# Optimization experiments

Hardware: AMD Instinct MI355X
Metric: run time of the kernel (lower is better)

Reference implementation:

```python
import jax, jax.numpy as jnp
import numpy as np
import math

FS = 44100.0
HOP = 256
N_BANDS = 24
KS_BUF = 768  # > max delay 44100/60 = 735 samples


def _lpc1(x, a):
    # order-1 all-pole (sample_wise_lpc with order 1, per-batch constant coeff):
    # y[n] = x[n] - a*y[n-1];  x: [B,N], a: [B]
    def step(yp, xt):
        y = xt - a * yp
        return y, y
    _, ys = jax.lax.scan(step, jnp.zeros_like(a), x.T)
    return ys.T


def _diff_ks(f0_frames, exc, l_b):
    # differentiable Karplus-Strong: fractional-delay loop + 2-tap damping filter.
    # f0_frames: [B,F] Hz, exc: [B,N], l_b: [B,F,2] (loop_coeff, loop_mix logits)
    B, N = exc.shape
    g = 0.999 * jax.nn.sigmoid(l_b[..., 0])   # loop gain in (0, 0.999)
    s = jax.nn.sigmoid(l_b[..., 1])           # loop-filter mix
    up = lambda p: jnp.repeat(p, HOP, axis=1)[:, :N]
    g_s, s_s = up(g), up(s)
    f0_s = up(jnp.clip(f0_frames, 60.0, None))
    D = jnp.clip(FS / f0_s, 2.0, 735.0)        # delay in samples
    Di = jnp.floor(D).astype(jnp.int32)
    fr = (D - Di).astype(exc.dtype)
    L = KS_BUF

    def step(carry, xs):
        buf, n = carry                         # buf: [B,L] circular delay line
        x_t, Di_t, fr_t, g_t, s_t = xs         # each [B]
        i1 = jnp.mod(n - Di_t, L)
        i2 = jnp.mod(n - Di_t - 1, L)
        i3 = jnp.mod(n - Di_t - 2, L)
        take = lambda i: jnp.take_along_axis(buf, i[:, None], axis=1)[:, 0]
        b1, b2, b3 = take(i1), take(i2), take(i3)
        z = (1.0 - fr_t) * b1 + fr_t * b2      # fractional-delay read y[n-D]
        z1 = (1.0 - fr_t) * b2 + fr_t * b3     # y[n-D-1]
        y = x_t + g_t * ((1.0 - s_t) * z + s_t * z1)
        buf = buf.at[:, jnp.mod(n, L)].set(y)
        return (buf, n + 1), y

    xs = (exc.T, Di.T, fr.T, g_s.T, s_s.T)
    init = (jnp.zeros((B, L), exc.dtype), jnp.int32(0))
    _, ys = jax.lax.scan(step, init, xs)
    return ys.T


def _body(x, body_gains):
    # bank of 24 two-pole resonators, log-spaced 80..8000 Hz, Q=10
    fc = jnp.geomspace(80.0, 8000.0, N_BANDS).astype(x.dtype)
    w = 2.0 * jnp.pi * fc / FS
    r = jnp.exp(-jnp.pi * fc / (10.0 * FS))
    a1 = -2.0 * r * jnp.cos(w)
    a2 = r * r
    b0 = 1.0 - r
    B = x.shape[0]

    def step(carry, xt):
        y1, y2 = carry                          # [B,24] each
        y = b0 * xt[:, None] - a1 * y1 - a2 * y2
        return (y, y1), jnp.sum(y * body_gains, axis=-1)

    init = (jnp.zeros((B, N_BANDS), x.dtype), jnp.zeros((B, N_BANDS), x.dtype))
    _, out = jax.lax.scan(step, init, x.T)
    return out.T


def _forward(excitation, pitch, w1, b1, w2, b2, excitation_gain, body_gains):
    B, _, N = excitation.shape
    h = jax.nn.relu(pitch @ w1.T + b1)
    mlp_out = h @ w2.T + b2                     # [B,3]
    loop_coeff = jnp.clip(mlp_out[:, 0], -2.0, 2.5)
    loop_mix = jnp.clip(mlp_out[:, 1], -2.5, 0.0)
    frames = N // HOP
    l_b = jnp.broadcast_to(jnp.stack([loop_coeff, loop_mix], -1)[:, None, :], (B, frames, 2))
    f0_frames = jnp.broadcast_to(pitch, (B, frames))
    exc_sq = (excitation * excitation_gain)[:, 0, :]
    f0_hz = jnp.clip(pitch[:, 0], 60.0, None)
    mult = jnp.clip(2.0 + 6.0 * (f0_hz - 60.0) / 600.0, 2.0, 8.0)
    cutoff = jnp.minimum(2.0 * jnp.pi * f0_hz * mult / FS, jnp.pi * 0.9)
    alpha = 1.0 - jnp.exp(-cutoff)
    exc_f = _lpc1(exc_sq * alpha[:, None], alpha - 1.0)   # pre-KS one-pole LP
    string = _diff_ks(f0_frames, exc_f, l_b)
    loop_post = jnp.clip(mlp_out[:, 2], -4.0, 4.0)
    cutoff_post = jnp.minimum(jnp.pi * jax.nn.sigmoid(loop_post), jnp.pi * 0.99)
    alpha_p = 1.0 - jnp.exp(-cutoff_post)
    string = _lpc1(string * alpha_p[:, None], alpha_p - 1.0)  # post one-pole LP
    out = _body(string, body_gains)
    return out[:, None, :], loop_coeff.mean(), loop_mix.mean(), loop_post.mean()


def setup_inputs():
    key = jax.random.key(0)
    k = jax.random.split(key, 6)
    B, N = 8, 32768
    excitation = jax.random.normal(k[0], (B, 1, N), dtype=jnp.float32)
    pitch = 60.0 + 600.0 * jax.random.uniform(k[1], (B, 1), dtype=jnp.float32)
    bnd1 = 0.1 * math.sqrt(6.0 / (1 + 16))   # xavier_uniform, gain 0.1
    bnd2 = 0.1 * math.sqrt(6.0 / (16 + 3))
    w1 = jax.random.uniform(k[2], (16, 1), jnp.float32, -bnd1, bnd1)
    b1 = jnp.zeros((16,), jnp.float32)
    w2 = jax.random.uniform(k[3], (3, 16), jnp.float32, -bnd2, bnd2)
    b2 = jnp.array([0.9, 0.0, 0.0], jnp.float32)
    excitation_gain = jnp.array(0.25, jnp.float32)
    body_gains = 0.006 * jnp.ones((1, N_BANDS), jnp.float32)
    return {"excitation": excitation, "pitch": pitch, "w1": w1, "b1": b1,
            "w2": w2, "b2": b2, "excitation_gain": excitation_gain,
            "body_gains": body_gains}


def reference(excitation, pitch, w1, b1, w2, b2, excitation_gain, body_gains):
    return _forward(excitation, pitch, w1, b1, w2, b2, excitation_gain, body_gains)
```

## Files before the change

### kernel.cpp

```cpp
#include <hip/hip_runtime.h>
#include <math.h>

#define NSAMP 32768
#define FS_F 44100.0f
#define PI_F 3.14159265358979323846f
#define T1 1024
#define FLAG_MAGIC 0x5A5A5A5A

struct BParams {
  float alpha, alpha_p;
  float fr, g, s;
  int Di;
  float lc, lm, lp;
};

__device__ inline float sigmoidf_(float x) { return 1.0f / (1.0f + expf(-x)); }

__device__ inline BParams compute_params(int b, const float* __restrict__ pitch,
                                         const float* __restrict__ w1,
                                         const float* __restrict__ b1,
                                         const float* __restrict__ w2,
                                         const float* __restrict__ b2) {
  BParams P;
  float p = pitch[b];
  float h[16];
#pragma unroll
  for (int i = 0; i < 16; ++i) {
    float v = fmaf(p, w1[i], b1[i]);
    h[i] = v > 0.0f ? v : 0.0f;
  }
  float m[3];
#pragma unroll
  for (int j = 0; j < 3; ++j) {
    float acc = b2[j];
#pragma unroll
    for (int i = 0; i < 16; ++i) acc = fmaf(h[i], w2[j * 16 + i], acc);
    m[j] = acc;
  }
  P.lc = fminf(fmaxf(m[0], -2.0f), 2.5f);
  P.lm = fminf(fmaxf(m[1], -2.5f), 0.0f);
  P.lp = fminf(fmaxf(m[2], -4.0f), 4.0f);
  P.g = 0.999f * sigmoidf_(P.lc);
  P.s = sigmoidf_(P.lm);
  float f0 = fmaxf(p, 60.0f);
  float D = fminf(fmaxf(FS_F / f0, 2.0f), 735.0f);
  int Di = (int)floorf(D);
  P.fr = D - (float)Di;
  P.Di = Di;
  float mult = fminf(fmaxf(2.0f + 6.0f * (f0 - 60.0f) / 600.0f, 2.0f), 8.0f);
  float cutoff = fminf(2.0f * PI_F * f0 * mult / FS_F, PI_F * 0.9f);
  P.alpha = 1.0f - expf(-cutoff);
  float cpost = fminf(PI_F * sigmoidf_(P.lp), PI_F * 0.99f);
  P.alpha_p = 1.0f - expf(-cpost);
  return P;
}

__device__ inline float rl63(float v) {
  return __int_as_float(__builtin_amdgcn_readlane(__float_as_int(v), 63));
}
__device__ inline float rlv(float v, int l) {
  return __int_as_float(__builtin_amdgcn_readlane(__float_as_int(v), l));
}
__device__ inline float shr1(float v, float bnd) {
  return __int_as_float(__builtin_amdgcn_update_dpp(
      __float_as_int(bnd), __float_as_int(v), 0x138 , 0xf, 0xf,
      false));
}

__device__ inline void barrier_lgkm() {
  asm volatile("s_waitcnt lgkmcnt(0)\n\ts_barrier" ::: "memory");
}

__device__ inline void band_coef(int k, float& a1, float& a2, float& b0) {
  float fc = 80.0f * exp2f((float)k * (6.64385618977472436f / 23.0f));
  float w = 2.0f * PI_F * fc / FS_F;
  float r = expf(-PI_F * fc / (10.0f * FS_F));
  a1 = -2.0f * r * cosf(w);
  a2 = r * r;
  b0 = 1.0f - r;
}

struct SCtx {
  const float* exc_b;
  float scale, c;
  float m1, m2, m4, m8, m16, m32, c512, c2048, c8lane, cgk;
  float vrun;
  int s1;
  float* lws;
};

__device__ inline void scan_seg(SCtx& SC, float* xbuf, int seg, bool write,
                                int t) {
  const int lane = t & 63, wid = t >> 6;
  const int rel0 = seg << 11;
  const int A = SC.s1 + rel0;
  __syncthreads();
  const int g0 = A + 8 * t;
  float4 xa = make_float4(0.f, 0.f, 0.f, 0.f);
  float4 xb = make_float4(0.f, 0.f, 0.f, 0.f);
  if (g0 >= 0 && g0 + 3 < NSAMP) xa = *(const float4*)&SC.exc_b[g0];
  if (g0 + 4 >= 0 && g0 + 7 < NSAMP) xb = *(const float4*)&SC.exc_b[g0 + 4];
  const float c = SC.c, scale = SC.scale;
  float S = 0.0f;
  S = fmaf(c, S, scale * xa.x); S = fmaf(c, S, scale * xa.y);
  S = fmaf(c, S, scale * xa.z); S = fmaf(c, S, scale * xa.w);
  S = fmaf(c, S, scale * xb.x); S = fmaf(c, S, scale * xb.y);
  S = fmaf(c, S, scale * xb.z); S = fmaf(c, S, scale * xb.w);
  float Sw = S, u;
  u = __shfl_up(Sw, 1);  if (lane >= 1)  Sw = fmaf(SC.m1, u, Sw);
  u = __shfl_up(Sw, 2);  if (lane >= 2)  Sw = fmaf(SC.m2, u, Sw);
  u = __shfl_up(Sw, 4);  if (lane >= 4)  Sw = fmaf(SC.m4, u, Sw);
  u = __shfl_up(Sw, 8);  if (lane >= 8)  Sw = fmaf(SC.m8, u, Sw);
  u = __shfl_up(Sw, 16); if (lane >= 16) Sw = fmaf(SC.m16, u, Sw);
  u = __shfl_up(Sw, 32); if (lane >= 32) Sw = fmaf(SC.m32, u, Sw);
  if (lane == 63) SC.lws[wid] = Sw;
  __syncthreads();
  float a0 = SC.lws[0], a1w = SC.lws[1], a2w = SC.lws[2], a3w = SC.lws[3];
  float carry = (wid == 1)   ? a0
                : (wid == 2) ? fmaf(SC.c512, a0, a1w)
                : (wid == 3) ? fmaf(SC.c512, fmaf(SC.c512, a0, a1w), a2w)
                             : 0.0f;
  float Sprev = __shfl_up(Sw, 1);
  float Sex = (lane == 0) ? 0.0f : Sprev;
  Sex = fmaf(SC.c8lane, carry, Sex);
  float v = fmaf(SC.cgk, SC.vrun, Sex);
  float4 ya, yb;
  v = fmaf(c, v, scale * xa.x); ya.x = v;
  v = fmaf(c, v, scale * xa.y); ya.y = v;
  v = fmaf(c, v, scale * xa.z); ya.z = v;
  v = fmaf(c, v, scale * xa.w); ya.w = v;
  v = fmaf(c, v, scale * xb.x); yb.x = v;
  v = fmaf(c, v, scale * xb.y); yb.y = v;
  v = fmaf(c, v, scale * xb.z); yb.z = v;
  v = fmaf(c, v, scale * xb.w); yb.w = v;
  if (write) {
    int o = (rel0 + 8 * t) & 8191;
    *(float4*)&xbuf[o] = ya;
    *(float4*)&xbuf[o + 4] = yb;
  }
  float tS = fmaf(SC.c512, fmaf(SC.c512, fmaf(SC.c512, a0, a1w), a2w), a3w);
  SC.vrun = fmaf(SC.c2048, SC.vrun, tS);
}

template <int KNUM>
__device__ void ks_slice2(SCtx& SC, float* __restrict__ yg, float* xbuf,
                          float* bnd, int t, int C, float c0w, float c1w,
                          float c2w, int s1, int n0, int end, int span,
                          int nseg) {
  const int lane = t & 63;
  const int wid = t >> 6;
  const int lq1 = (C - 1) - (KNUM - 1) * 64;
  const int W = n0 - s1;

  if (KNUM <= 3) {
    float yp[KNUM], xC[KNUM], xN[KNUM], xN2[KNUM];
    float p1 = 0.f, p2 = 0.f;
    int rel = 0;
#pragma unroll
    for (int k = 0; k < KNUM; ++k) {
      yp[k] = 0.f; xC[k] = 0.f; xN[k] = 0.f; xN2[k] = 0.f;
    }
    for (int s = 0; s < nseg; ++s) {
      barrier_lgkm();
      if (wid == 0) {
        if (s == 0) {
#pragma unroll
          for (int k = 0; k < KNUM; ++k) {
            int i = lane + (k << 6);
            xC[k] = xbuf[i];
            xN[k] = xbuf[C + i];
            xN2[k] = xbuf[2 * C + i];
          }
        }
        int fence = (s + 1) << 11;
        if (fence > span) fence = span;
        while (rel + C <= W && rel < fence) {
          float b2v[KNUM], b3v[KNUM];
#pragma unroll
          for (int k = 0; k < KNUM; ++k)
            b2v[k] = shr1(yp[k], (k == 0) ? p1 : rl63(yp[k - 1]));
#pragma unroll
          for (int k = 0; k < KNUM; ++k)
            b3v[k] = shr1(b2v[k], (k == 0) ? p2 : rlv(yp[k - 1], 62));
          float p1n = rlv(yp[KNUM - 1], lq1);
          float p2n = rlv(b2v[KNUM - 1], lq1);
#pragma unroll
          for (int k = 0; k < KNUM; ++k)
            yp[k] = fmaf(c0w, yp[k],
                         fmaf(c2w, b3v[k], fmaf(c1w, b2v[k], xC[k])));
          p1 = p1n;
          p2 = p2n;
#pragma unroll
          for (int k = 0; k < KNUM; ++k) {
            xC[k] = xN[k];
            xN[k] = xN2[k];
            xN2[k] = xbuf[(rel + 3 * C + lane + (k << 6)) & 8191];
          }
          rel += C;
        }
        while (rel < fence) {
          float b2v[KNUM], b3v[KNUM];
#pragma unroll
          for (int k = 0; k < KNUM; ++k)
            b2v[k] = shr1(yp[k], (k == 0) ? p1 : rl63(yp[k - 1]));
#pragma unroll
          for (int k = 0; k < KNUM; ++k)
            b3v[k] = shr1(b2v[k], (k == 0) ? p2 : rlv(yp[k - 1], 62));
          float p1n = rlv(yp[KNUM - 1], lq1);
          float p2n = rlv(b2v[KNUM - 1], lq1);
#pragma unroll
          for (int k = 0; k < KNUM; ++k)
            yp[k] = fmaf(c0w, yp[k],
                         fmaf(c2w, b3v[k], fmaf(c1w, b2v[k], xC[k])));
          p1 = p1n;
          p2 = p2n;
#pragma unroll
          for (int k = 0; k < KNUM; ++k) {
            int i = lane + (k << 6);
            int n = s1 + rel + i;
            bool okl = (k < KNUM - 1) || (lane <= lq1);
            if (okl && n >= n0 && n < end) yg[n] = yp[k];
          }
#pragma unroll
          for (int k = 0; k < KNUM; ++k) {
            xC[k] = xN[k];
            xN[k] = xN2[k];
            xN2[k] = xbuf[(rel + 3 * C + lane + (k << 6)) & 8191];
          }
          rel += C;
        }
      }
      barrier_lgkm();
      int ls = s + 3;
      if (ls < nseg) scan_seg(SC, xbuf, ls, true, t);
    }
  } else {
    constexpr int SPW = (KNUM + 3) / 4;
    const int kbase = wid * SPW;
    float yp[SPW], xC[SPW], xN[SPW], xN2[SPW];
    int rel = 0, par = 0;
#pragma unroll
    for (int kk = 0; kk < SPW; ++kk) {
      yp[kk] = 0.f; xC[kk] = 0.f; xN[kk] = 0.f; xN2[kk] = 0.f;
    }
    for (int s = 0; s < nseg; ++s) {
      barrier_lgkm();
      if (s == 0) {
#pragma unroll
        for (int kk = 0; kk < SPW; ++kk) {
          int k = kbase + kk;
          if (k < KNUM) {
            int i = lane + (k << 6);
            xC[kk] = xbuf[i];
            xN[kk] = xbuf[C + i];
            xN2[kk] = xbuf[2 * C + i];
          }
        }
      }
      int fence = (s + 1) << 11;
      if (fence > span) fence = span;
      while (rel < fence) {
        const bool lean = (rel + C <= W);
        barrier_lgkm();
        const int rb = par << 5, wb = rb ^ 32;
        float pbA = 0.f, pbB = 0.f;
        if (kbase == 0) {
          pbA = bnd[rb + 24];
          pbB = bnd[rb + 25];
        } else if (kbase < KNUM) {
          pbA = bnd[rb + (kbase - 1) * 2];
          pbB = bnd[rb + (kbase - 1) * 2 + 1];
        }
        float b2v[SPW], b3v[SPW];
#pragma unroll
        for (int kk = 0; kk < SPW; ++kk) {
          int k = kbase + kk;
          if (k < KNUM)
            b2v[kk] = shr1(yp[kk], (kk == 0) ? pbA : rl63(yp[kk - 1]));
        }
#pragma unroll
        for (int kk = 0; kk < SPW; ++kk) {
          int k = kbase + kk;
          if (k < KNUM)
            b3v[kk] = shr1(b2v[kk], (kk == 0) ? pbB : rlv(yp[kk - 1], 62));
        }
        float p1n = 0.f, p2n = 0.f;
        const bool ownLast = (KNUM - 1 >= kbase) && (KNUM - 1 < kbase + SPW);
        if (ownLast) {
          p1n = rlv(yp[KNUM - 1 - kbase], lq1);
          p2n = rlv(b2v[KNUM - 1 - kbase], lq1);
        }
#pragma unroll
        for (int kk = 0; kk < SPW; ++kk) {
          int k = kbase + kk;
          if (k < KNUM)
            yp[kk] = fmaf(c0w, yp[kk],
                          fmaf(c2w, b3v[kk], fmaf(c1w, b2v[kk], xC[kk])));
        }
        if (!lean) {
#pragma unroll
          for (int kk = 0; kk < SPW; ++kk) {
            int k = kbase + kk;
            if (k < KNUM) {
              int i = lane + (k << 6);
              int n = s1 + rel + i;
              bool okl = (k < KNUM - 1) || (lane <= lq1);
              if (okl && n >= n0 && n < end) yg[n] = yp[kk];
            }
          }
        }
#pragma unroll
        for (int kk = 0; kk < SPW; ++kk) {
          int k = kbase + kk;
          if (k < KNUM) {
            float h63 = rlv(yp[kk], 63);
            float h62 = rlv(yp[kk], 62);
            if (lane == 0) {
              bnd[wb + k * 2] = h63;
              bnd[wb + k * 2 + 1] = h62;
            }
          }
        }
        if (ownLast && lane == 0) {
          bnd[wb + 24] = p1n;
          bnd[wb + 25] = p2n;
        }
#pragma unroll
        for (int kk = 0; kk < SPW; ++kk) {
          int k = kbase + kk;
          if (k < KNUM) {
            xC[kk] = xN[kk];
            xN[kk] = xN2[kk];
            xN2[kk] = xbuf[(rel + 3 * C + lane + (k << 6)) & 8191];
          }
        }
        rel += C;
        par ^= 1;
      }
      barrier_lgkm();
      int ls = s + 3;
      if (ls < nseg) scan_seg(SC, xbuf, ls, true, t);
    }
  }
}

__device__ inline void lpc_lds(const float* __restrict__ xg,
                               float* __restrict__ sl, int s2, int nt, int lim,
                               float scale, float c, int t, float* lws) {
  const int lane = t & 63, wid = t >> 6;
  float c2v = c * c, c4 = c2v * c2v, c8 = c4 * c4;
  float m1 = c8, m2 = m1 * m1, m4 = m2 * m2, m8 = m4 * m4, m16 = m8 * m8,
        m32 = m16 * m16;
  float c512 = m32 * m32;
  float c2048 = c512 * c512;
  c2048 *= c2048;
  float l2c = log2f(c);
  float c8lane = exp2f((float)(8 * lane) * l2c);
  float cgk = exp2f((float)(8 * t) * l2c);
  float vrun = 0.0f;
  for (int tile = 0; tile < nt; ++tile) {
    __syncthreads();
    int g0 = s2 + (tile << 11) + 8 * t;
    float4 xa = make_float4(0.f, 0.f, 0.f, 0.f);
    float4 xb = make_float4(0.f, 0.f, 0.f, 0.f);
    if (g0 + 3 < lim) xa = *(const float4*)&xg[g0];
    if (g0 + 7 < lim) xb = *(const float4*)&xg[g0 + 4];
    float S = 0.0f;
    S = fmaf(c, S, scale * xa.x); S = fmaf(c, S, scale * xa.y);
    S = fmaf(c, S, scale * xa.z); S = fmaf(c, S, scale * xa.w);
    S = fmaf(c, S, scale * xb.x); S = fmaf(c, S, scale * xb.y);
    S = fmaf(c, S, scale * xb.z); S = fmaf(c, S, scale * xb.w);
    float Sw = S, u;
    u = __shfl_up(Sw, 1);  if (lane >= 1)  Sw = fmaf(m1, u, Sw);
    u = __shfl_up(Sw, 2);  if (lane >= 2)  Sw = fmaf(m2, u, Sw);
    u = __shfl_up(Sw, 4);  if (lane >= 4)  Sw = fmaf(m4, u, Sw);
    u = __shfl_up(Sw, 8);  if (lane >= 8)  Sw = fmaf(m8, u, Sw);
    u = __shfl_up(Sw, 16); if (lane >= 16) Sw = fmaf(m16, u, Sw);
    u = __shfl_up(Sw, 32); if (lane >= 32) Sw = fmaf(m32, u, Sw);
    if (lane == 63) lws[wid] = Sw;
    __syncthreads();
    float a0 = lws[0], a1w = lws[1], a2w = lws[2], a3w = lws[3];
    float carry = (wid == 1)   ? a0
                  : (wid == 2) ? fmaf(c512, a0, a1w)
                  : (wid == 3) ? fmaf(c512, fmaf(c512, a0, a1w), a2w)
                               : 0.0f;
    float Sprev = __shfl_up(Sw, 1);
    float Sex = (lane == 0) ? 0.0f : Sprev;
    Sex = fmaf(c8lane, carry, Sex);
    float v = fmaf(cgk, vrun, Sex);
    int o = g0 - s2;
    float4 ya, yb;
    v = fmaf(c, v, scale * xa.x); ya.x = v;
    v = fmaf(c, v, scale * xa.y); ya.y = v;
    v = fmaf(c, v, scale * xa.z); ya.z = v;
    v = fmaf(c, v, scale * xa.w); ya.w = v;
    v = fmaf(c, v, scale * xb.x); yb.x = v;
    v = fmaf(c, v, scale * xb.y); yb.y = v;
    v = fmaf(c, v, scale * xb.z); yb.z = v;
    v = fmaf(c, v, scale * xb.w); yb.w = v;
    *(float4*)&sl[o] = ya;
    *(float4*)&sl[o + 4] = yb;
    float tS = fmaf(c512, fmaf(c512, fmaf(c512, a0, a1w), a2w), a3w);
    vrun = fmaf(c2048, vrun, tS);
  }
}

__device__ inline void ks_phase(int b, int q, const BParams& P,
                                const float* __restrict__ exc, float scale0,
                                float* __restrict__ buf1, float* xbuf,
                                float* bnd, float* lws, int t) {
  const int C = P.Di;
  const int n0 = q << 10;
  float lg = -logf(P.g);
  int Wp = (int)ceilf(10.5f / fmaxf(lg, 1e-6f));
  if (Wp > 64) Wp = 64;
  if (Wp < 4) Wp = 4;
  int W = Wp * C;
  if (W > n0) W = n0;
  W = (W + 3) & ~3;
  const int s1 = n0 - W;
  const int span = W + T1;
  const int end = n0 + T1;
  const int nseg = (span + 2047) >> 11;
  float* yg = buf1 + (size_t)b * NSAMP;

  SCtx SC;
  SC.exc_b = exc + (size_t)b * NSAMP;
  SC.c = 1.0f - P.alpha;
  SC.scale = scale0 * P.alpha;
  {
    float c = SC.c;
    float c2v = c * c, c4 = c2v * c2v, c8 = c4 * c4;
    SC.m1 = c8;
    SC.m2 = SC.m1 * SC.m1;
    SC.m4 = SC.m2 * SC.m2;
    SC.m8 = SC.m4 * SC.m4;
    SC.m16 = SC.m8 * SC.m8;
    SC.m32 = SC.m16 * SC.m16;
    SC.c512 = SC.m32 * SC.m32;
    float c1024 = SC.c512 * SC.c512;
    SC.c2048 = c1024 * c1024;
    float l2c = log2f(c);
    SC.c8lane = exp2f((float)(8 * (t & 63)) * l2c);
    SC.cgk = exp2f((float)(8 * t) * l2c);
  }
  SC.vrun = 0.0f;
  SC.s1 = s1;
  SC.lws = lws;

  if (s1 > 0) scan_seg(SC, xbuf, -1, false, t);
  scan_seg(SC, xbuf, 0, true, t);
  scan_seg(SC, xbuf, 1, true, t);
  scan_seg(SC, xbuf, 2, true, t);
  if (t < 64) bnd[t] = 0.0f;

  const float c0w = P.g * (1.0f - P.s) * (1.0f - P.fr);
  const float c1w = P.g * ((1.0f - P.s) * P.fr + P.s * (1.0f - P.fr));
  const float c2w = P.g * P.s * P.fr;
  switch ((C + 63) >> 6) {
    case 2:  ks_slice2<2>(SC, yg, xbuf, bnd, t, C, c0w, c1w, c2w, s1, n0, end, span, nseg); break;
    case 3:  ks_slice2<3>(SC, yg, xbuf, bnd, t, C, c0w, c1w, c2w, s1, n0, end, span, nseg); break;
    case 4:  ks_slice2<4>(SC, yg, xbuf, bnd, t, C, c0w, c1w, c2w, s1, n0, end, span, nseg); break;
    case 5:  ks_slice2<5>(SC, yg, xbuf, bnd, t, C, c0w, c1w, c2w, s1, n0, end, span, nseg); break;
    case 6:  ks_slice2<6>(SC, yg, xbuf, bnd, t, C, c0w, c1w, c2w, s1, n0, end, span, nseg); break;
    case 7:  ks_slice2<7>(SC, yg, xbuf, bnd, t, C, c0w, c1w, c2w, s1, n0, end, span, nseg); break;
    case 8:  ks_slice2<8>(SC, yg, xbuf, bnd, t, C, c0w, c1w, c2w, s1, n0, end, span, nseg); break;
    case 9:  ks_slice2<9>(SC, yg, xbuf, bnd, t, C, c0w, c1w, c2w, s1, n0, end, span, nseg); break;
    case 10: ks_slice2<10>(SC, yg, xbuf, bnd, t, C, c0w, c1w, c2w, s1, n0, end, span, nseg); break;
    case 11: ks_slice2<11>(SC, yg, xbuf, bnd, t, C, c0w, c1w, c2w, s1, n0, end, span, nseg); break;
    default: ks_slice2<12>(SC, yg, xbuf, bnd, t, C, c0w, c1w, c2w, s1, n0, end, span, nseg); break;
  }
}

__device__ inline void body_phase(int b, int q, const BParams& P,
                                  const float* __restrict__ gains,
                                  const float* __restrict__ buf1,
                                  float* __restrict__ out, float* sl,
                                  float* lws, float (*lc0)[8],
                                  float (*lc1)[8], int t) {
  const int lane = t & 63, wid = t >> 6;
  const int n0 = q << 10;
  const int base = n0 - 4096;
  int s2 = base - 256;
  if (s2 < 0) s2 = 0;
  const int end = n0 + 1024;
  const int nt = (end - s2 + 2047) >> 11;

  lpc_lds(buf1 + (size_t)b * NSAMP, sl, s2, nt, end, P.alpha_p,
          1.0f - P.alpha_p, t, lws);
  __syncthreads();

  const int tb = base + 20 * t;
  float4 acc[5];
#pragma unroll
  for (int i = 0; i < 5; ++i) acc[i] = make_float4(0.f, 0.f, 0.f, 0.f);

  for (int g = 0; g < 3; ++g) {
    float A1[8], A2[8], B0[8], GN[8];
#pragma unroll
    for (int j = 0; j < 8; ++j) {
      int k = g * 8 + j;
      band_coef(k, A1[j], A2[j], B0[j]);
      GN[j] = gains[k];
    }
    float cv0[8], cv1[8];
#pragma unroll
    for (int j = 0; j < 8; ++j) cv0[j] = cv1[j] = 0.f;
    for (int i = 0; i < 5; ++i) {
      int n = tb + 4 * i;
      float4 xv = make_float4(0.f, 0.f, 0.f, 0.f);
      if (n >= 0) xv = *(const float4*)&sl[n - s2];
#pragma unroll
      for (int e = 0; e < 4; ++e) {
        float xi = e == 0 ? xv.x : e == 1 ? xv.y : e == 2 ? xv.z : xv.w;
#pragma unroll
        for (int j = 0; j < 8; ++j) {
          float nc = fmaf(B0[j], xi, -fmaf(A1[j], cv0[j], A2[j] * cv1[j]));
          cv1[j] = cv0[j];
          cv0[j] = nc;
        }
      }
    }
    float Q00[8], Q01[8], Q10[8], Q11[8];
    float K00[8], K01[8], K10[8], K11[8];
#pragma unroll
    for (int j = 0; j < 8; ++j) {
      Q00[j] = -A1[j]; Q01[j] = -A2[j]; Q10[j] = 1.f; Q11[j] = 0.f;
    }
    for (int sq = 0; sq < 2; ++sq) {
#pragma unroll
      for (int j = 0; j < 8; ++j) {
        float n00 = fmaf(Q00[j], Q00[j], Q01[j] * Q10[j]);
        float n01 = fmaf(Q00[j], Q01[j], Q01[j] * Q11[j]);
        float n10 = fmaf(Q10[j], Q00[j], Q11[j] * Q10[j]);
        float n11 = fmaf(Q10[j], Q01[j], Q11[j] * Q11[j]);
        Q00[j] = n00; Q01[j] = n01; Q10[j] = n10; Q11[j] = n11;
      }
    }
#pragma unroll
    for (int j = 0; j < 8; ++j) {
      K00[j] = Q00[j]; K01[j] = Q01[j]; K10[j] = Q10[j]; K11[j] = Q11[j];
    }
    for (int sq = 0; sq < 2; ++sq) {
#pragma unroll
      for (int j = 0; j < 8; ++j) {
        float n00 = fmaf(Q00[j], Q00[j], Q01[j] * Q10[j]);
        float n01 = fmaf(Q00[j], Q01[j], Q01[j] * Q11[j]);
        float n10 = fmaf(Q10[j], Q00[j], Q11[j] * Q10[j]);
        float n11 = fmaf(Q10[j], Q01[j], Q11[j] * Q11[j]);
        Q00[j] = n00; Q01[j] = n01; Q10[j] = n10; Q11[j] = n11;
      }
    }
    float T00[8], T01[8], T10[8], T11[8];
#pragma unroll
    for (int j = 0; j < 8; ++j) {
      float n00 = fmaf(Q00[j], K00[j], Q01[j] * K10[j]);
      float n01 = fmaf(Q00[j], K01[j], Q01[j] * K11[j]);
      float n10 = fmaf(Q10[j], K00[j], Q11[j] * K10[j]);
      float n11 = fmaf(Q10[j], K01[j], Q11[j] * K11[j]);
      Q00[j] = n00; Q01[j] = n01; Q10[j] = n10; Q11[j] = n11;
      T00[j] = n00; T01[j] = n01; T10[j] = n10; T11[j] = n11;
    }
    for (int off = 1; off <= 32; off <<= 1) {
#pragma unroll
      for (int j = 0; j < 8; ++j) {
        float u0 = __shfl_up(cv0[j], off);
        float u1 = __shfl_up(cv1[j], off);
        if (lane >= off) {
          float nc0 = fmaf(Q00[j], u0, fmaf(Q01[j], u1, cv0[j]));
          float nc1 = fmaf(Q10[j], u0, fmaf(Q11[j], u1, cv1[j]));
          cv0[j] = nc0;
          cv1[j] = nc1;
        }
        float n00 = fmaf(Q00[j], Q00[j], Q01[j] * Q10[j]);
        float n01 = fmaf(Q00[j], Q01[j], Q01[j] * Q11[j]);
        float n10 = fmaf(Q10[j], Q00[j], Q11[j] * Q10[j]);
        float n11 = fmaf(Q10[j], Q01[j], Q11[j] * Q11[j]);
        Q00[j] = n00; Q01[j] = n01; Q10[j] = n10; Q11[j] = n11;
      }
    }
    __syncthreads();
    if (lane == 63) {
#pragma unroll
      for (int j = 0; j < 8; ++j) {
        lc0[wid][j] = cv0[j];
        lc1[wid][j] = cv1[j];
      }
    }
    __syncthreads();
    float car0[8], car1[8];
#pragma unroll
    for (int j = 0; j < 8; ++j) car0[j] = car1[j] = 0.f;
    for (int v = 0; v < wid; ++v) {
#pragma unroll
      for (int j = 0; j < 8; ++j) {
        float n0c = fmaf(Q00[j], car0[j], fmaf(Q01[j], car1[j], lc0[v][j]));
        float n1c = fmaf(Q10[j], car0[j], fmaf(Q11[j], car1[j], lc1[v][j]));
        car0[j] = n0c;
        car1[j] = n1c;
      }
    }
    float R00[8], R01[8], R10[8], R11[8];
#pragma unroll
    for (int j = 0; j < 8; ++j) {
      R00[j] = 1.f; R01[j] = 0.f; R10[j] = 0.f; R11[j] = 1.f;
    }
    for (int bit = 0; bit < 6; ++bit) {
      bool on = (lane >> bit) & 1;
#pragma unroll
      for (int j = 0; j < 8; ++j) {
        if (on) {
          float n00 = fmaf(T00[j], R00[j], T01[j] * R10[j]);
          float n01 = fmaf(T00[j], R01[j], T01[j] * R11[j]);
          float n10 = fmaf(T10[j], R00[j], T11[j] * R10[j]);
          float n11 = fmaf(T10[j], R01[j], T11[j] * R11[j]);
          R00[j] = n00; R01[j] = n01; R10[j] = n10; R11[j] = n11;
        }
        float s00 = fmaf(T00[j], T00[j], T01[j] * T10[j]);
        float s01 = fmaf(T00[j], T01[j], T01[j] * T11[j]);
        float s10 = fmaf(T10[j], T00[j], T11[j] * T10[j]);
        float s11 = fmaf(T10[j], T01[j], T11[j] * T11[j]);
        T00[j] = s00; T01[j] = s01; T10[j] = s10; T11[j] = s11;
      }
    }
    float y1[8], y2[8];
#pragma unroll
    for (int j = 0; j < 8; ++j) {
      float e0 = __shfl_up(cv0[j], 1);
      float e1 = __shfl_up(cv1[j], 1);
      if (lane == 0) { e0 = 0.f; e1 = 0.f; }
      y1[j] = fmaf(R00[j], car0[j], fmaf(R01[j], car1[j], e0));
      y2[j] = fmaf(R10[j], car0[j], fmaf(R11[j], car1[j], e1));
    }
    if (tb + 20 > n0) {
      for (int i = 0; i < 5; ++i) {
        float4 xv = *(const float4*)&sl[tb - s2 + 4 * i];
        float4 ov = acc[i];
#pragma unroll
        for (int e = 0; e < 4; ++e) {
          float xi = e == 0 ? xv.x : e == 1 ? xv.y : e == 2 ? xv.z : xv.w;
          float a = 0.f;
#pragma unroll
          for (int j = 0; j < 8; ++j) {
            float yv = fmaf(B0[j], xi, -fmaf(A1[j], y1[j], A2[j] * y2[j]));
            y2[j] = y1[j];
            y1[j] = yv;
            a = fmaf(GN[j], yv, a);
          }
          if (e == 0) ov.x += a;
          else if (e == 1) ov.y += a;
          else if (e == 2) ov.z += a;
          else ov.w += a;
        }
        acc[i] = ov;
      }
    }
  }
  if (tb + 20 > n0) {
    float* outb = out + (size_t)b * NSAMP;
#pragma unroll
    for (int i = 0; i < 5; ++i) {
      int n = tb + 4 * i;
      if (n >= n0) *(float4*)&outb[n] = acc[i];
    }
  }
}

__global__ void __launch_bounds__(256, 1) synth_all(
    const float* __restrict__ exc, const float* __restrict__ pitch,
    const float* __restrict__ w1, const float* __restrict__ b1,
    const float* __restrict__ w2, const float* __restrict__ b2,
    const float* __restrict__ eg, const float* __restrict__ gains,
    float* __restrict__ buf1, int* __restrict__ flags,
    float* __restrict__ out) {
  const int blk = blockIdx.x;
  const int b = blk >> 5, q = blk & 31;
  const int t = threadIdx.x;
  __shared__ __align__(16) float smem[8264];

  BParams P = compute_params(b, pitch, w1, b1, w2, b2);
  if (blk == 0 && t < 64) {
    int bb = (t < 8) ? t : 0;
    BParams Q = compute_params(bb, pitch, w1, b1, w2, b2);
    float slc = 0.f, slm = 0.f, slp = 0.f;
    for (int i = 0; i < 8; ++i) {
      slc += rlv(Q.lc, i);
      slm += rlv(Q.lm, i);
      slp += rlv(Q.lp, i);
    }
    if (t == 0) {
      out[8 * NSAMP + 0] = slc / 8.0f;
      out[8 * NSAMP + 1] = slm / 8.0f;
      out[8 * NSAMP + 2] = slp / 8.0f;
    }
  }

  ks_phase(b, q, P, exc, eg[0], buf1, smem, smem + 8192, smem + 8256, t);
  __syncthreads();

  const int n0 = q << 10;
  int s2 = n0 - 4096 - 256;
  if (s2 < 0) s2 = 0;
  const int qlo = s2 >> 10;
  if (t == 0) {
    __hip_atomic_store(&flags[blk], FLAG_MAGIC, __ATOMIC_RELEASE,
                       __HIP_MEMORY_SCOPE_AGENT);
    for (int f = qlo; f < q; ++f) {
      while (__hip_atomic_load(&flags[b * 32 + f], __ATOMIC_ACQUIRE,
                               __HIP_MEMORY_SCOPE_AGENT) != FLAG_MAGIC) {
        __builtin_amdgcn_s_sleep(8);
      }
    }
  }
  __syncthreads();

  body_phase(b, q, P, gains, buf1, out, smem, smem + 6144,
             (float(*)[8])(smem + 6152), (float(*)[8])(smem + 6184), t);
}

extern "C" void kernel_launch(void* const* d_in, const int* in_sizes, int n_in,
                              void* d_out, int out_size, void* d_ws, size_t ws_size,
                              hipStream_t stream) {
  const float* exc = (const float*)d_in[0];
  const float* pitch = (const float*)d_in[1];
  const float* w1 = (const float*)d_in[2];
  const float* b1 = (const float*)d_in[3];
  const float* w2 = (const float*)d_in[4];
  const float* b2 = (const float*)d_in[5];
  const float* eg = (const float*)d_in[6];
  const float* bg = (const float*)d_in[7];
  float* out = (float*)d_out;
  float* buf1 = (float*)d_ws;
  int* flags = (int*)(buf1 + 8 * NSAMP);

  hipLaunchKernelGGL(synth_all, dim3(256), dim3(256), 0, stream, exc, pitch,
                     w1, b1, w2, b2, eg, bg, buf1, flags, out);
}
```

Baseline: 133.5 us.

## Run Karplus-Strong loop on one wave and overlap LPC scan on another

The Karplus-Strong recurrence now always runs inside wave 0, which holds all delay-line slices in registers. This replaces the multi-wave path for long delays, which traded boundary values through LDS with a block barrier every step. Wave 1 computes the order-1 LPC prescan of upcoming segments with a per-wave shuffle scan and prefetched global loads, so it overlaps with the recurrence instead of interleaving block-wide scans. The first four segment loads are issued up front, and the boundary LDS scratch is removed. The cost is that long-delay batches do serial per-lane work on one wave, and waves 2 and 3 sit idle during this phase.

```diff
diff --git a/kernel.cpp b/kernel.cpp
--- a/kernel.cpp
+++ b/kernel.cpp
@@ -89,17 +89,19 @@
   float* lws;
 };
 
-__device__ inline void scan_seg(SCtx& SC, float* xbuf, int seg, bool write,
-                                int t) {
+__device__ inline void ld2(const float* __restrict__ p, int g0, float4& a,
+                           float4& b) {
+  a = make_float4(0.f, 0.f, 0.f, 0.f);
+  b = make_float4(0.f, 0.f, 0.f, 0.f);
+  if (g0 >= 0 && g0 + 3 < NSAMP) a = *(const float4*)&p[g0];
+  if (g0 + 4 >= 0 && g0 + 7 < NSAMP) b = *(const float4*)&p[g0 + 4];
+}
+
+__device__ inline void scan_seg_pre(SCtx& SC, float* xbuf, int seg, bool write,
+                                    int t, float4 xa, float4 xb) {
   const int lane = t & 63, wid = t >> 6;
   const int rel0 = seg << 11;
-  const int A = SC.s1 + rel0;
-  __syncthreads();
-  const int g0 = A + 8 * t;
-  float4 xa = make_float4(0.f, 0.f, 0.f, 0.f);
-  float4 xb = make_float4(0.f, 0.f, 0.f, 0.f);
-  if (g0 >= 0 && g0 + 3 < NSAMP) xa = *(const float4*)&SC.exc_b[g0];
-  if (g0 + 4 >= 0 && g0 + 7 < NSAMP) xb = *(const float4*)&SC.exc_b[g0 + 4];
+  barrier_lgkm();
   const float c = SC.c, scale = SC.scale;
   float S = 0.0f;
   S = fmaf(c, S, scale * xa.x); S = fmaf(c, S, scale * xa.y);
@@ -114,7 +116,7 @@
   u = __shfl_up(Sw, 16); if (lane >= 16) Sw = fmaf(SC.m16, u, Sw);
   u = __shfl_up(Sw, 32); if (lane >= 32) Sw = fmaf(SC.m32, u, Sw);
   if (lane == 63) SC.lws[wid] = Sw;
-  __syncthreads();
+  barrier_lgkm();
   float a0 = SC.lws[0], a1w = SC.lws[1], a2w = SC.lws[2], a3w = SC.lws[3];
   float carry = (wid == 1)   ? a0
                 : (wid == 2) ? fmaf(SC.c512, a0, a1w)
@@ -142,205 +144,221 @@
   SC.vrun = fmaf(SC.c2048, SC.vrun, tS);
 }
 
+__device__ inline void w1_load(const float* __restrict__ xg, int s1, int seg,
+                               int lane, float4* pf) {
+  const int base = s1 + (seg << 11) + (lane << 5);
+#pragma unroll
+  for (int i = 0; i < 8; ++i) {
+    const int g = base + 4 * i;
+    float4 v = make_float4(0.f, 0.f, 0.f, 0.f);
+    if (g >= 0 && g + 3 < NSAMP) v = *(const float4*)&xg[g];
+    pf[i] = v;
+  }
+}
+
 template <int KNUM>
-__device__ void ks_slice2(SCtx& SC, float* __restrict__ yg, float* xbuf,
-                          float* bnd, int t, int C, float c0w, float c1w,
-                          float c2w, int s1, int n0, int end, int span,
-                          int nseg) {
-  const int lane = t & 63;
-  const int wid = t >> 6;
+__device__ void ks_wave0(float* __restrict__ yg, const float* xbuf, int lane,
+                         int C, float c0w, float c1w, float c2w, int s1,
+                         int n0, int end, int span, int nseg) {
   const int lq1 = (C - 1) - (KNUM - 1) * 64;
   const int W = n0 - s1;
-
-  if (KNUM <= 3) {
-    float yp[KNUM], xC[KNUM], xN[KNUM], xN2[KNUM];
-    float p1 = 0.f, p2 = 0.f;
-    int rel = 0;
-#pragma unroll
-    for (int k = 0; k < KNUM; ++k) {
-      yp[k] = 0.f; xC[k] = 0.f; xN[k] = 0.f; xN2[k] = 0.f;
-    }
+  float yp[KNUM], xC[KNUM], xN[KNUM], xN2[KNUM];
+  float p1 = 0.f, p2 = 0.f;
+  int rel = 0;
+#pragma unroll
+  for (int k = 0; k < KNUM; ++k) {
+    yp[k] = 0.f; xC[k] = 0.f; xN[k] = 0.f; xN2[k] = 0.f;
+  }
+  for (int s = 0; s < nseg; ++s) {
+    barrier_lgkm();
+    if (s == 0) {
+#pragma unroll
+      for (int k = 0; k < KNUM; ++k) {
+        int i = lane + (k << 6);
+        xC[k] = xbuf[i];
+        xN[k] = xbuf[C + i];
+        xN2[k] = xbuf[2 * C + i];
+      }
+    }
+    int fence = (s + 1) << 11;
+    if (fence > span) fence = span;
+    while (rel + C <= W && rel < fence) {
+      float b2v[KNUM], b3v[KNUM];
+#pragma unroll
+      for (int k = 0; k < KNUM; ++k)
+        b2v[k] = shr1(yp[k], (k == 0) ? p1 : rl63(yp[k - 1]));
+#pragma unroll
+      for (int k = 0; k < KNUM; ++k)
+        b3v[k] = shr1(b2v[k], (k == 0) ? p2 : rlv(yp[k - 1], 62));
+      float p1n = rlv(yp[KNUM - 1], lq1);
+      float p2n = rlv(b2v[KNUM - 1], lq1);
+#pragma unroll
+      for (int k = 0; k < KNUM; ++k)
+        yp[k] = fmaf(c0w, yp[k], fmaf(c2w, b3v[k], fmaf(c1w, b2v[k], xC[k])));
+      p1 = p1n;
+      p2 = p2n;
+#pragma unroll
+      for (int k = 0; k < KNUM; ++k) {
+        xC[k] = xN[k];
+        xN[k] = xN2[k];
+        xN2[k] = xbuf[(rel + 3 * C + lane + (k << 6)) & 8191];
+      }
+      rel += C;
+    }
+    while (rel < fence) {
+      float b2v[KNUM], b3v[KNUM];
+#pragma unroll
+      for (int k = 0; k < KNUM; ++k)
+        b2v[k] = shr1(yp[k], (k == 0) ? p1 : rl63(yp[k - 1]));
+#pragma unroll
+      for (int k = 0; k < KNUM; ++k)
+        b3v[k] = shr1(b2v[k], (k == 0) ? p2 : rlv(yp[k - 1], 62));
+      float p1n = rlv(yp[KNUM - 1], lq1);
+      float p2n = rlv(b2v[KNUM - 1], lq1);
+#pragma unroll
+      for (int k = 0; k < KNUM; ++k)
+        yp[k] = fmaf(c0w, yp[k], fmaf(c2w, b3v[k], fmaf(c1w, b2v[k], xC[k])));
+      p1 = p1n;
+      p2 = p2n;
+#pragma unroll
+      for (int k = 0; k < KNUM; ++k) {
+        int i = lane + (k << 6);
+        int n = s1 + rel + i;
+        bool okl = (k < KNUM - 1) || (lane <= lq1);
+        if (okl && n >= n0 && n < end) yg[n] = yp[k];
+      }
+#pragma unroll
+      for (int k = 0; k < KNUM; ++k) {
+        xC[k] = xN[k];
+        xN[k] = xN2[k];
+        xN2[k] = xbuf[(rel + 3 * C + lane + (k << 6)) & 8191];
+      }
+      rel += C;
+    }
+  }
+}
+
+__device__ inline void ks_phase(int b, int q, const BParams& P,
+                                const float* __restrict__ exc, float scale0,
+                                float* __restrict__ buf1, float* xbuf,
+                                float* lws, int t) {
+  const int C = P.Di;
+  const int n0 = q << 10;
+  float lg = -logf(P.g);
+  int Wp = (int)ceilf(10.5f / fmaxf(lg, 1e-6f));
+  if (Wp > 64) Wp = 64;
+  if (Wp < 4) Wp = 4;
+  int W = Wp * C;
+  if (W > n0) W = n0;
+  W = (W + 3) & ~3;
+  const int s1 = n0 - W;
+  const int span = W + T1;
+  const int end = n0 + T1;
+  const int nseg = (span + 2047) >> 11;
+  float* yg = buf1 + (size_t)b * NSAMP;
+
+  SCtx SC;
+  SC.exc_b = exc + (size_t)b * NSAMP;
+  SC.c = 1.0f - P.alpha;
+  SC.scale = scale0 * P.alpha;
+  {
+    float c = SC.c;
+    float c2v = c * c, c4 = c2v * c2v, c8 = c4 * c4;
+    SC.m1 = c8;
+    SC.m2 = SC.m1 * SC.m1;
+    SC.m4 = SC.m2 * SC.m2;
+    SC.m8 = SC.m4 * SC.m4;
+    SC.m16 = SC.m8 * SC.m8;
+    SC.m32 = SC.m16 * SC.m16;
+    SC.c512 = SC.m32 * SC.m32;
+    float c1024 = SC.c512 * SC.c512;
+    SC.c2048 = c1024 * c1024;
+    float l2c = log2f(c);
+    SC.c8lane = exp2f((float)(8 * (t & 63)) * l2c);
+    SC.cgk = exp2f((float)(8 * t) * l2c);
+  }
+  SC.vrun = 0.0f;
+  SC.s1 = s1;
+  SC.lws = lws;
+
+  const float* xg = SC.exc_b;
+  float4 pA0, pB0, pA1, pB1, pA2, pB2, pA3, pB3;
+  ld2(xg, s1 - 2048 + 8 * t, pA0, pB0);
+  ld2(xg, s1 + 8 * t, pA1, pB1);
+  ld2(xg, s1 + 2048 + 8 * t, pA2, pB2);
+  ld2(xg, s1 + 4096 + 8 * t, pA3, pB3);
+  scan_seg_pre(SC, xbuf, -1, false, t, pA0, pB0);
+  scan_seg_pre(SC, xbuf, 0, true, t, pA1, pB1);
+  scan_seg_pre(SC, xbuf, 1, true, t, pA2, pB2);
+  scan_seg_pre(SC, xbuf, 2, true, t, pA3, pB3);
+
+  const float c0w = P.g * (1.0f - P.s) * (1.0f - P.fr);
+  const float c1w = P.g * ((1.0f - P.s) * P.fr + P.s * (1.0f - P.fr));
+  const float c2w = P.g * P.s * P.fr;
+  const int lane = t & 63, wid = t >> 6;
+
+  if (wid == 0) {
+    switch ((C + 63) >> 6) {
+      case 2:  ks_wave0<2>(yg, xbuf, lane, C, c0w, c1w, c2w, s1, n0, end, span, nseg); break;
+      case 3:  ks_wave0<3>(yg, xbuf, lane, C, c0w, c1w, c2w, s1, n0, end, span, nseg); break;
+      case 4:  ks_wave0<4>(yg, xbuf, lane, C, c0w, c1w, c2w, s1, n0, end, span, nseg); break;
+      case 5:  ks_wave0<5>(yg, xbuf, lane, C, c0w, c1w, c2w, s1, n0, end, span, nseg); break;
+      case 6:  ks_wave0<6>(yg, xbuf, lane, C, c0w, c1w, c2w, s1, n0, end, span, nseg); break;
+      case 7:  ks_wave0<7>(yg, xbuf, lane, C, c0w, c1w, c2w, s1, n0, end, span, nseg); break;
+      case 8:  ks_wave0<8>(yg, xbuf, lane, C, c0w, c1w, c2w, s1, n0, end, span, nseg); break;
+      case 9:  ks_wave0<9>(yg, xbuf, lane, C, c0w, c1w, c2w, s1, n0, end, span, nseg); break;
+      case 10: ks_wave0<10>(yg, xbuf, lane, C, c0w, c1w, c2w, s1, n0, end, span, nseg); break;
+      case 11: ks_wave0<11>(yg, xbuf, lane, C, c0w, c1w, c2w, s1, n0, end, span, nseg); break;
+      default: ks_wave0<12>(yg, xbuf, lane, C, c0w, c1w, c2w, s1, n0, end, span, nseg); break;
+    }
+  } else if (wid == 1) {
+    const float c = SC.c, scale = SC.scale;
+    const float n1 = SC.m4, n2 = SC.m8, n4 = SC.m16, n8 = SC.m32;
+    const float n16 = SC.c512, n32 = SC.c512 * SC.c512;
+    const float c2048 = SC.c2048;
+    const float c32lane = exp2f((float)(lane << 5) * log2f(c));
+    float vrun = SC.vrun;
+    float4 pf[8];
+    w1_load(xg, s1, 3, lane, pf);
     for (int s = 0; s < nseg; ++s) {
       barrier_lgkm();
-      if (wid == 0) {
-        if (s == 0) {
-#pragma unroll
-          for (int k = 0; k < KNUM; ++k) {
-            int i = lane + (k << 6);
-            xC[k] = xbuf[i];
-            xN[k] = xbuf[C + i];
-            xN2[k] = xbuf[2 * C + i];
-          }
+      const int ls = s + 3;
+      if (ls < nseg) {
+        float S = 0.0f;
+#pragma unroll
+        for (int i = 0; i < 8; ++i) {
+          S = fmaf(c, S, scale * pf[i].x);
+          S = fmaf(c, S, scale * pf[i].y);
+          S = fmaf(c, S, scale * pf[i].z);
+          S = fmaf(c, S, scale * pf[i].w);
         }
-        int fence = (s + 1) << 11;
-        if (fence > span) fence = span;
-        while (rel + C <= W && rel < fence) {
-          float b2v[KNUM], b3v[KNUM];
-#pragma unroll
-          for (int k = 0; k < KNUM; ++k)
-            b2v[k] = shr1(yp[k], (k == 0) ? p1 : rl63(yp[k - 1]));
-#pragma unroll
-          for (int k = 0; k < KNUM; ++k)
-            b3v[k] = shr1(b2v[k], (k == 0) ? p2 : rlv(yp[k - 1], 62));
-          float p1n = rlv(yp[KNUM - 1], lq1);
-          float p2n = rlv(b2v[KNUM - 1], lq1);
-#pragma unroll
-          for (int k = 0; k < KNUM; ++k)
-            yp[k] = fmaf(c0w, yp[k],
-                         fmaf(c2w, b3v[k], fmaf(c1w, b2v[k], xC[k])));
-          p1 = p1n;
-          p2 = p2n;
-#pragma unroll
-          for (int k = 0; k < KNUM; ++k) {
-            xC[k] = xN[k];
-            xN[k] = xN2[k];
-            xN2[k] = xbuf[(rel + 3 * C + lane + (k << 6)) & 8191];
-          }
-          rel += C;
+        float Sw = S, u;
+        u = __shfl_up(Sw, 1);  if (lane >= 1)  Sw = fmaf(n1, u, Sw);
+        u = __shfl_up(Sw, 2);  if (lane >= 2)  Sw = fmaf(n2, u, Sw);
+        u = __shfl_up(Sw, 4);  if (lane >= 4)  Sw = fmaf(n4, u, Sw);
+        u = __shfl_up(Sw, 8);  if (lane >= 8)  Sw = fmaf(n8, u, Sw);
+        u = __shfl_up(Sw, 16); if (lane >= 16) Sw = fmaf(n16, u, Sw);
+        u = __shfl_up(Sw, 32); if (lane >= 32) Sw = fmaf(n32, u, Sw);
+        float tot = rlv(Sw, 63);
+        float Sex = __shfl_up(Sw, 1);
+        if (lane == 0) Sex = 0.0f;
+        float v = fmaf(c32lane, vrun, Sex);
+        const int o = ((ls << 11) & 8191) + (lane << 5);
+#pragma unroll
+        for (int i = 0; i < 8; ++i) {
+          float4 y;
+          v = fmaf(c, v, scale * pf[i].x); y.x = v;
+          v = fmaf(c, v, scale * pf[i].y); y.y = v;
+          v = fmaf(c, v, scale * pf[i].z); y.z = v;
+          v = fmaf(c, v, scale * pf[i].w); y.w = v;
+          *(float4*)&xbuf[o + 4 * i] = y;
         }
-        while (rel < fence) {
-          float b2v[KNUM], b3v[KNUM];
-#pragma unroll
-          for (int k = 0; k < KNUM; ++k)
-            b2v[k] = shr1(yp[k], (k == 0) ? p1 : rl63(yp[k - 1]));
-#pragma unroll
-          for (int k = 0; k < KNUM; ++k)
-            b3v[k] = shr1(b2v[k], (k == 0) ? p2 : rlv(yp[k - 1], 62));
-          float p1n = rlv(yp[KNUM - 1], lq1);
-          float p2n = rlv(b2v[KNUM - 1], lq1);
-#pragma unroll
-          for (int k = 0; k < KNUM; ++k)
-            yp[k] = fmaf(c0w, yp[k],
-                         fmaf(c2w, b3v[k], fmaf(c1w, b2v[k], xC[k])));
-          p1 = p1n;
-          p2 = p2n;
-#pragma unroll
-          for (int k = 0; k < KNUM; ++k) {
-            int i = lane + (k << 6);
-            int n = s1 + rel + i;
-            bool okl = (k < KNUM - 1) || (lane <= lq1);
-            if (okl && n >= n0 && n < end) yg[n] = yp[k];
-          }
-#pragma unroll
-          for (int k = 0; k < KNUM; ++k) {
-            xC[k] = xN[k];
-            xN[k] = xN2[k];
-            xN2[k] = xbuf[(rel + 3 * C + lane + (k << 6)) & 8191];
-          }
-          rel += C;
-        }
-      }
-      barrier_lgkm();
-      int ls = s + 3;
-      if (ls < nseg) scan_seg(SC, xbuf, ls, true, t);
+        vrun = fmaf(c2048, vrun, tot);
+        w1_load(xg, s1, ls + 1, lane, pf);
+      }
     }
   } else {
-    constexpr int SPW = (KNUM + 3) / 4;
-    const int kbase = wid * SPW;
-    float yp[SPW], xC[SPW], xN[SPW], xN2[SPW];
-    int rel = 0, par = 0;
-#pragma unroll
-    for (int kk = 0; kk < SPW; ++kk) {
-      yp[kk] = 0.f; xC[kk] = 0.f; xN[kk] = 0.f; xN2[kk] = 0.f;
-    }
-    for (int s = 0; s < nseg; ++s) {
-      barrier_lgkm();
-      if (s == 0) {
-#pragma unroll
-        for (int kk = 0; kk < SPW; ++kk) {
-          int k = kbase + kk;
-          if (k < KNUM) {
-            int i = lane + (k << 6);
-            xC[kk] = xbuf[i];
-            xN[kk] = xbuf[C + i];
-            xN2[kk] = xbuf[2 * C + i];
-          }
-        }
-      }
-      int fence = (s + 1) << 11;
-      if (fence > span) fence = span;
-      while (rel < fence) {
-        const bool lean = (rel + C <= W);
-        barrier_lgkm();
-        const int rb = par << 5, wb = rb ^ 32;
-        float pbA = 0.f, pbB = 0.f;
-        if (kbase == 0) {
-          pbA = bnd[rb + 24];
-          pbB = bnd[rb + 25];
-        } else if (kbase < KNUM) {
-          pbA = bnd[rb + (kbase - 1) * 2];
-          pbB = bnd[rb + (kbase - 1) * 2 + 1];
-        }
-        float b2v[SPW], b3v[SPW];
-#pragma unroll
-        for (int kk = 0; kk < SPW; ++kk) {
-          int k = kbase + kk;
-          if (k < KNUM)
-            b2v[kk] = shr1(yp[kk], (kk == 0) ? pbA : rl63(yp[kk - 1]));
-        }
-#pragma unroll
-        for (int kk = 0; kk < SPW; ++kk) {
-          int k = kbase + kk;
-          if (k < KNUM)
-            b3v[kk] = shr1(b2v[kk], (kk == 0) ? pbB : rlv(yp[kk - 1], 62));
-        }
-        float p1n = 0.f, p2n = 0.f;
-        const bool ownLast = (KNUM - 1 >= kbase) && (KNUM - 1 < kbase + SPW);
-        if (ownLast) {
-          p1n = rlv(yp[KNUM - 1 - kbase], lq1);
-          p2n = rlv(b2v[KNUM - 1 - kbase], lq1);
-        }
-#pragma unroll
-        for (int kk = 0; kk < SPW; ++kk) {
-          int k = kbase + kk;
-          if (k < KNUM)
-            yp[kk] = fmaf(c0w, yp[kk],
-                          fmaf(c2w, b3v[kk], fmaf(c1w, b2v[kk], xC[kk])));
-        }
-        if (!lean) {
-#pragma unroll
-          for (int kk = 0; kk < SPW; ++kk) {
-            int k = kbase + kk;
-            if (k < KNUM) {
-              int i = lane + (k << 6);
-              int n = s1 + rel + i;
-              bool okl = (k < KNUM - 1) || (lane <= lq1);
-              if (okl && n >= n0 && n < end) yg[n] = yp[kk];
-            }
-          }
-        }
-#pragma unroll
-        for (int kk = 0; kk < SPW; ++kk) {
-          int k = kbase + kk;
-          if (k < KNUM) {
-            float h63 = rlv(yp[kk], 63);
-            float h62 = rlv(yp[kk], 62);
-            if (lane == 0) {
-              bnd[wb + k * 2] = h63;
-              bnd[wb + k * 2 + 1] = h62;
-            }
-          }
-        }
-        if (ownLast && lane == 0) {
-          bnd[wb + 24] = p1n;
-          bnd[wb + 25] = p2n;
-        }
-#pragma unroll
-        for (int kk = 0; kk < SPW; ++kk) {
-          int k = kbase + kk;
-          if (k < KNUM) {
-            xC[kk] = xN[kk];
-            xN[kk] = xN2[kk];
-            xN2[kk] = xbuf[(rel + 3 * C + lane + (k << 6)) & 8191];
-          }
-        }
-        rel += C;
-        par ^= 1;
-      }
-      barrier_lgkm();
-      int ls = s + 3;
-      if (ls < nseg) scan_seg(SC, xbuf, ls, true, t);
-    }
+    for (int s = 0; s < nseg; ++s) barrier_lgkm();
   }
 }
 
@@ -405,73 +423,6 @@
   }
 }
 
-__device__ inline void ks_phase(int b, int q, const BParams& P,
-                                const float* __restrict__ exc, float scale0,
-                                float* __restrict__ buf1, float* xbuf,
-                                float* bnd, float* lws, int t) {
-  const int C = P.Di;
-  const int n0 = q << 10;
-  float lg = -logf(P.g);
-  int Wp = (int)ceilf(10.5f / fmaxf(lg, 1e-6f));
-  if (Wp > 64) Wp = 64;
-  if (Wp < 4) Wp = 4;
-  int W = Wp * C;
-  if (W > n0) W = n0;
-  W = (W + 3) & ~3;
-  const int s1 = n0 - W;
-  const int span = W + T1;
-  const int end = n0 + T1;
-  const int nseg = (span + 2047) >> 11;
-  float* yg = buf1 + (size_t)b * NSAMP;
-
-  SCtx SC;
-  SC.exc_b = exc + (size_t)b * NSAMP;
-  SC.c = 1.0f - P.alpha;
-  SC.scale = scale0 * P.alpha;
-  {
-    float c = SC.c;
-    float c2v = c * c, c4 = c2v * c2v, c8 = c4 * c4;
-    SC.m1 = c8;
-    SC.m2 = SC.m1 * SC.m1;
-    SC.m4 = SC.m2 * SC.m2;
-    SC.m8 = SC.m4 * SC.m4;
-    SC.m16 = SC.m8 * SC.m8;
-    SC.m32 = SC.m16 * SC.m16;
-    SC.c512 = SC.m32 * SC.m32;
-    float c1024 = SC.c512 * SC.c512;
-    SC.c2048 = c1024 * c1024;
-    float l2c = log2f(c);
-    SC.c8lane = exp2f((float)(8 * (t & 63)) * l2c);
-    SC.cgk = exp2f((float)(8 * t) * l2c);
-  }
-  SC.vrun = 0.0f;
-  SC.s1 = s1;
-  SC.lws = lws;
-
-  if (s1 > 0) scan_seg(SC, xbuf, -1, false, t);
-  scan_seg(SC, xbuf, 0, true, t);
-  scan_seg(SC, xbuf, 1, true, t);
-  scan_seg(SC, xbuf, 2, true, t);
-  if (t < 64) bnd[t] = 0.0f;
-
-  const float c0w = P.g * (1.0f - P.s) * (1.0f - P.fr);
-  const float c1w = P.g * ((1.0f - P.s) * P.fr + P.s * (1.0f - P.fr));
-  const float c2w = P.g * P.s * P.fr;
-  switch ((C + 63) >> 6) {
-    case 2:  ks_slice2<2>(SC, yg, xbuf, bnd, t, C, c0w, c1w, c2w, s1, n0, end, span, nseg); break;
-    case 3:  ks_slice2<3>(SC, yg, xbuf, bnd, t, C, c0w, c1w, c2w, s1, n0, end, span, nseg); break;
-    case 4:  ks_slice2<4>(SC, yg, xbuf, bnd, t, C, c0w, c1w, c2w, s1, n0, end, span, nseg); break;
-    case 5:  ks_slice2<5>(SC, yg, xbuf, bnd, t, C, c0w, c1w, c2w, s1, n0, end, span, nseg); break;
-    case 6:  ks_slice2<6>(SC, yg, xbuf, bnd, t, C, c0w, c1w, c2w, s1, n0, end, span, nseg); break;
-    case 7:  ks_slice2<7>(SC, yg, xbuf, bnd, t, C, c0w, c1w, c2w, s1, n0, end, span, nseg); break;
-    case 8:  ks_slice2<8>(SC, yg, xbuf, bnd, t, C, c0w, c1w, c2w, s1, n0, end, span, nseg); break;
-    case 9:  ks_slice2<9>(SC, yg, xbuf, bnd, t, C, c0w, c1w, c2w, s1, n0, end, span, nseg); break;
-    case 10: ks_slice2<10>(SC, yg, xbuf, bnd, t, C, c0w, c1w, c2w, s1, n0, end, span, nseg); break;
-    case 11: ks_slice2<11>(SC, yg, xbuf, bnd, t, C, c0w, c1w, c2w, s1, n0, end, span, nseg); break;
-    default: ks_slice2<12>(SC, yg, xbuf, bnd, t, C, c0w, c1w, c2w, s1, n0, end, span, nseg); break;
-  }
-}
-
 __device__ inline void body_phase(int b, int q, const BParams& P,
                                   const float* __restrict__ gains,
                                   const float* __restrict__ buf1,
@@ -676,7 +627,7 @@
   const int blk = blockIdx.x;
   const int b = blk >> 5, q = blk & 31;
   const int t = threadIdx.x;
-  __shared__ __align__(16) float smem[8264];
+  __shared__ __align__(16) float smem[8200];
 
   BParams P = compute_params(b, pitch, w1, b1, w2, b2);
   if (blk == 0 && t < 64) {
@@ -695,7 +646,7 @@
     }
   }
 
-  ks_phase(b, q, P, exc, eg[0], buf1, smem, smem + 8192, smem + 8256, t);
+  ks_phase(b, q, P, exc, eg[0], buf1, smem, smem + 8192, t);
   __syncthreads();
 
   const int n0 = q << 10;
```

Result: faster. 119.1 us (-10.8%).
